# Kernel optimization log

Measured on AMD Instinct MI355X. Metric: run time of the kernel, lower is better.

Reference implementation:

```python
import jax, jax.numpy as jnp
import numpy as np

JACCARD_THRESH = 0.5
NEG_POS = 3
VAR0, VAR1 = 0.1, 0.2

def point_form(priors):
    # center form (cx,cy,w,h) -> corner form (x1,y1,x2,y2)
    return jnp.concatenate([priors[:, :2] - priors[:, 2:] / 2,
                            priors[:, :2] + priors[:, 2:] / 2], axis=1)

def jaccard(a, b):
    # a: [G,4] corner-form gt, b: [P,4] corner-form priors -> IoU [G,P]
    lt = jnp.maximum(a[:, None, :2], b[None, :, :2])
    rb = jnp.minimum(a[:, None, 2:], b[None, :, 2:])
    wh = jnp.maximum(rb - lt, 0.0)
    inter = wh[..., 0] * wh[..., 1]
    area_a = ((a[:, 2] - a[:, 0]) * (a[:, 3] - a[:, 1]))[:, None]
    area_b = ((b[:, 2] - b[:, 0]) * (b[:, 3] - b[:, 1]))[None, :]
    return inter / (area_a + area_b - inter)

def encode(matched, priors):
    # matched: [P,4] corner form; priors: [P,4] center form
    g_cxcy = ((matched[:, :2] + matched[:, 2:]) / 2 - priors[:, :2]) / (VAR0 * priors[:, 2:])
    g_wh = jnp.log((matched[:, 2:] - matched[:, :2]) / priors[:, 2:]) / VAR1
    return jnp.concatenate([g_cxcy, g_wh], axis=1)

def match_one(truths, labels, priors_c, priors_p):
    # truths: [G,4], labels: [G] -> loc_t [P,4], conf_t [P]
    G = truths.shape[0]
    overlaps = jaccard(truths, priors_p)            # [G,P]
    best_prior_idx = jnp.argmax(overlaps, axis=1)   # [G]
    best_truth_overlap = jnp.max(overlaps, axis=0)  # [P]
    best_truth_idx = jnp.argmax(overlaps, axis=0)   # [P]
    # force each gt's best prior to match that gt
    best_truth_overlap = best_truth_overlap.at[best_prior_idx].set(2.0)
    best_truth_idx = best_truth_idx.at[best_prior_idx].set(jnp.arange(G))
    matched = truths[best_truth_idx]                # [P,4]
    conf = labels[best_truth_idx].astype(jnp.int32) + 1
    conf = jnp.where(best_truth_overlap < JACCARD_THRESH, 0, conf)
    return encode(matched, priors_c), conf

def smooth_l1(x, y):
    d = jnp.abs(x - y)
    return jnp.where(d < 1.0, 0.5 * d * d, d - 0.5)

def setup_inputs() -> dict:
    key = jax.random.key(0)
    B, P, G, C = 64, 24564, 32, 81
    k1, k2, k3, k4, k5, k6, k7 = jax.random.split(key, 7)
    loc_data = jax.random.normal(k1, (B, P, 4), jnp.float32)
    conf_data = jax.random.normal(k2, (B, P, C), jnp.float32)
    # center-form priors with positive w,h
    cxcy = jax.random.uniform(k3, (P, 2), minval=0.0, maxval=1.0)
    wh = jax.random.uniform(k4, (P, 2), minval=0.05, maxval=0.5)
    dbox_list = jnp.concatenate([cxcy, wh], axis=1).astype(jnp.float32)
    # valid corner-form gt boxes + float class label in last column
    gc = jax.random.uniform(k5, (B, G, 2), minval=0.1, maxval=0.9)
    gwh = jax.random.uniform(k6, (B, G, 2), minval=0.1, maxval=0.4)
    boxes = jnp.clip(jnp.concatenate([gc - gwh / 2, gc + gwh / 2], axis=-1), 0.0, 1.0)
    labels = jax.random.randint(k7, (B, G), 0, C - 1).astype(jnp.float32)
    targets = jnp.concatenate([boxes, labels[..., None]], axis=-1).astype(jnp.float32)
    return {"loc_data": loc_data, "conf_data": conf_data,
            "dbox_list": dbox_list, "targets": targets}

def reference(loc_data, conf_data, dbox_list, targets):
    B, P, C = conf_data.shape
    priors_p = point_form(dbox_list)
    loc_t, conf_t = jax.vmap(match_one, in_axes=(0, 0, None, None))(
        targets[..., :4], targets[..., 4], dbox_list, priors_p)
    loc_t = jax.lax.stop_gradient(loc_t)           # detached in torch
    pos = conf_t > 0                               # [B,P]
    # localization smooth-L1, summed over positives
    loss_l = jnp.sum(jnp.where(pos[..., None], smooth_l1(loc_data, loc_t), 0.0))
    # per-box cross entropy
    logp = jax.nn.log_softmax(conf_data, axis=-1)  # [B,P,C]
    ce = -jnp.take_along_axis(logp, conf_t[..., None], axis=-1)[..., 0]  # [B,P]
    # hard negative mining via double argsort rank trick
    loss_for_rank = jnp.where(pos, 0.0, ce)
    loss_idx = jnp.argsort(-loss_for_rank, axis=1)
    idx_rank = jnp.argsort(loss_idx, axis=1)
    num_pos = jnp.sum(pos, axis=1, keepdims=True)  # [B,1]
    num_neg = jnp.minimum(num_pos * NEG_POS, P)
    neg = idx_rank < num_neg
    loss_c = jnp.sum(jnp.where(pos | neg, ce, 0.0))
    N = jnp.sum(num_pos).astype(loc_data.dtype)
    return loss_c / N, loss_l / N
```

## Files before the change

kernel.cpp:

```cpp
#include <hip/hip_runtime.h>
#include <math.h>


constexpr float kJT = 0.5f;
constexpr float kV0 = 0.1f;
constexpr float kV1 = 0.2f;

__global__ void init_ws_kernel(unsigned int* ws, int nwords) {
  int i = blockIdx.x * blockDim.x + threadIdx.x;
  if (i < nwords) ws[i] = 0u;
}

__global__ void match_kernel(const float* __restrict__ dbox,
                             const float* __restrict__ targets,
                             float* __restrict__ bto,
                             int* __restrict__ bti,
                             unsigned long long* __restrict__ gt_best,
                             int P, int G) {
#pragma clang fp contract(off)
  constexpr int NP = 6;
  const int b = blockIdx.y;
  const int tid = threadIdx.x;
  const int lane = tid & 63;
  const int p0 = blockIdx.x * (NP * 256);

  __shared__ float tx1[64], ty1[64], tx2[64], ty2[64], tarea[64];
  __shared__ unsigned long long sbest[64];
  if (tid < G) {
    const float* t = targets + ((size_t)b * G + tid) * 5;
    float x1 = t[0], y1 = t[1], x2 = t[2], y2 = t[3];
    tx1[tid] = x1; ty1[tid] = y1; tx2[tid] = x2; ty2[tid] = y2;
    tarea[tid] = (x2 - x1) * (y2 - y1);
    sbest[tid] = 0ull;
  }
  __syncthreads();

  float px1[NP], py1[NP], px2[NP], py2[NP], pa[NP], bov[NP];
  int bg[NP], pidx[NP];
  bool val[NP];
#pragma unroll
  for (int i = 0; i < NP; ++i) {
    int p = p0 + i * 256 + tid;
    pidx[i] = p; val[i] = (p < P);
    bov[i] = -1.0f; bg[i] = 0;
    if (val[i]) {
      const float* d = dbox + (size_t)p * 4;
      float cx = d[0], cy = d[1], w = d[2], h = d[3];
      px1[i] = cx - w * 0.5f; py1[i] = cy - h * 0.5f;
      px2[i] = cx + w * 0.5f; py2[i] = cy + h * 0.5f;
      pa[i] = (px2[i] - px1[i]) * (py2[i] - py1[i]);
    }
  }

  for (int g = 0; g < G; ++g) {
    float x1 = tx1[g], y1 = ty1[g], x2 = tx2[g], y2 = ty2[g], ta = tarea[g];
    unsigned long long lk = 0ull;
#pragma unroll
    for (int i = 0; i < NP; ++i) {
      if (!val[i]) continue;
      float lx = fmaxf(x1, px1[i]);
      float ly = fmaxf(y1, py1[i]);
      float rx = fminf(x2, px2[i]);
      float ry = fminf(y2, py2[i]);
      float w = fmaxf(rx - lx, 0.0f);
      float h = fmaxf(ry - ly, 0.0f);
      float inter = w * h;
      float ov = inter / (ta + pa[i] - inter);
      if (ov > bov[i]) { bov[i] = ov; bg[i] = g; }
      unsigned long long key =
          ((unsigned long long)__float_as_uint(ov) << 32) | (unsigned)(~(unsigned)pidx[i]);
      lk = (key > lk) ? key : lk;
    }
#pragma unroll
    for (int off = 32; off > 0; off >>= 1) {
      unsigned long long o = __shfl_xor(lk, off);
      lk = (o > lk) ? o : lk;
    }
    if (lane == 0) atomicMax(&sbest[g], lk);
  }
  __syncthreads();
  if (tid < G) atomicMax(&gt_best[(size_t)b * G + tid], sbest[tid]);

#pragma unroll
  for (int i = 0; i < NP; ++i) {
    if (val[i]) {
      bto[(size_t)b * P + pidx[i]] = bov[i];
      bti[(size_t)b * P + pidx[i]] = bg[i];
    }
  }
}

__global__ void force_kernel(const unsigned long long* __restrict__ gt_best,
                             float* __restrict__ bto, int* __restrict__ bti,
                             int P, int G, int B) {
  int b = blockIdx.x * blockDim.x + threadIdx.x;
  if (b >= B) return;
  for (int g = 0; g < G; ++g) {
    unsigned long long key = gt_best[(size_t)b * G + g];
    unsigned p = ~(unsigned)(key & 0xFFFFFFFFull);
    bto[(size_t)b * P + p] = 2.0f;
    bti[(size_t)b * P + p] = g;
  }
}

__global__ __launch_bounds__(256)
void ce_kernel(const float* __restrict__ conf,
               const float* __restrict__ loc,
               const float* __restrict__ dbox,
               const float* __restrict__ targets,
               const float* __restrict__ bto,
               const int* __restrict__ bti,
               float* __restrict__ lfr,
               int* __restrict__ num_pos,
               float* __restrict__ loss_l_b,
               float* __restrict__ ce_pos_b,
               int P, int C, int G) {
  constexpr int NC = 21;
  const int b = blockIdx.y;
  const int p0 = blockIdx.x * 64;
  const int rows = min(64, P - p0);
  const int nflt = rows * C;

  __shared__ float srow[64 * 84];
  __shared__ float s_ll, s_ce;
  __shared__ int s_np;
  if (threadIdx.x == 0) { s_ll = 0.0f; s_ce = 0.0f; s_np = 0; }

  const float* base = conf + ((size_t)b * P + p0) * (size_t)C;
  if (((uintptr_t)base & 15) == 0) {
    const float4* src4 = (const float4*)base;
    float4* dst4 = (float4*)srow;
    const int n4 = nflt >> 2;
    for (int i = threadIdx.x; i < n4; i += 256) dst4[i] = src4[i];
    for (int i = (n4 << 2) + threadIdx.x; i < nflt; i += 256) srow[i] = base[i];
  } else {
    for (int i = threadIdx.x; i < nflt; i += 256) srow[i] = base[i];
  }
  __syncthreads();

  const int lane = threadIdx.x & 63;
  const int wave = threadIdx.x >> 6;
  const int group = lane >> 2;
  const int sub = lane & 3;
  const int r = wave * 16 + group;

  if (r < rows) {
    const int p = p0 + r;
    const float* row = srow + r * C;
    float v[NC];
#pragma unroll
    for (int j = 0; j < NC; ++j) {
      int idx = j * 4 + sub;
      v[j] = (idx < C) ? row[idx] : -INFINITY;
    }
    float m = v[0];
#pragma unroll
    for (int j = 1; j < NC; ++j) m = fmaxf(m, v[j]);
    m = fmaxf(m, __shfl_xor(m, 1));
    m = fmaxf(m, __shfl_xor(m, 2));

    float s = 0.0f;
#pragma unroll
    for (int j = 0; j < NC; ++j) s += __expf(v[j] - m);
    s += __shfl_xor(s, 1);
    s += __shfl_xor(s, 2);
    float lse = m + __logf(s);

    float ov = bto[(size_t)b * P + p];
    int g = bti[(size_t)b * P + p];
    float label = targets[((size_t)b * G + g) * 5 + 4];
    int cls = (ov < kJT) ? 0 : ((int)label + 1);

    int cj = cls >> 2, cs = cls & 3;
    float vsel = 0.0f;
#pragma unroll
    for (int j = 0; j < NC; ++j) vsel = (j == cj) ? v[j] : vsel;
    float xt = (sub == cs) ? vsel : 0.0f;
    xt += __shfl_xor(xt, 1);
    xt += __shfl_xor(xt, 2);

    float ce = lse - xt;
    bool pos = cls > 0;

    if (sub == 0) {
      lfr[(size_t)b * P + p] = pos ? 0.0f : ce;
      if (pos) {
        const float* t = targets + ((size_t)b * G + g) * 5;
        float mx1 = t[0], my1 = t[1], mx2 = t[2], my2 = t[3];
        const float* d = dbox + (size_t)p * 4;
        float cx = d[0], cy = d[1], pw = d[2], ph = d[3];
        float gcx = ((mx1 + mx2) * 0.5f - cx) / (kV0 * pw);
        float gcy = ((my1 + my2) * 0.5f - cy) / (kV0 * ph);
        float gw = logf((mx2 - mx1) / pw) / kV1;
        float gh = logf((my2 - my1) / ph) / kV1;
        const float* lp = loc + ((size_t)b * P + p) * 4;
        float tloc[4] = {gcx, gcy, gw, gh};
        float ll = 0.0f;
        for (int k = 0; k < 4; ++k) {
          float dd = fabsf(lp[k] - tloc[k]);
          ll += (dd < 1.0f) ? (0.5f * dd * dd) : (dd - 0.5f);
        }
        atomicAdd(&s_ll, ll);
        atomicAdd(&s_ce, ce);
        atomicAdd(&s_np, 1);
      }
    }
  }
  __syncthreads();
  if (threadIdx.x == 0 && s_np > 0) {
    atomicAdd(&num_pos[b], s_np);
    atomicAdd(&loss_l_b[b], s_ll);
    atomicAdd(&ce_pos_b[b], s_ce);
  }
}

__global__ __launch_bounds__(1024)
void topk_kernel(const float* __restrict__ lfr,
                 const int* __restrict__ num_pos,
                 float* __restrict__ topk_sum, int P) {
  const int b = blockIdx.x;
  const int tid = threadIdx.x;
  const int lane = tid & 63;
  const int wave = tid >> 6;
  const int nthr = blockDim.x;
  const int nwav = nthr >> 6;
  const float* v = lfr + (size_t)b * P;
  int K = num_pos[b] * 3;
  if (K > P) K = P;

  __shared__ int wcnt[16][4];
  __shared__ unsigned s_prefix;
  __shared__ int s_krem;
  __shared__ float wred[16];

  if (K <= 0) {
    if (tid == 0) topk_sum[b] = 0.0f;
    return;
  }

  unsigned prefix = 0u, mask = 0u;
  int Krem = K;
  for (int shift = 30; shift >= 0; shift -= 2) {
    int c0 = 0, c1 = 0, c2 = 0, c3 = 0;
    for (int p = tid; p < P; p += nthr) {
      unsigned key = __float_as_uint(v[p]);
      bool act = (key & mask) == prefix;
      int d = (key >> shift) & 3;
      c0 += __popcll(__ballot(act & (d == 0)));
      c1 += __popcll(__ballot(act & (d == 1)));
      c2 += __popcll(__ballot(act & (d == 2)));
      c3 += __popcll(__ballot(act & (d == 3)));
    }
    if (lane == 0) {
      wcnt[wave][0] = c0; wcnt[wave][1] = c1;
      wcnt[wave][2] = c2; wcnt[wave][3] = c3;
    }
    __syncthreads();
    if (tid == 0) {
      int t[4] = {0, 0, 0, 0};
      for (int w = 0; w < nwav; ++w)
        for (int d = 0; d < 4; ++d) t[d] += wcnt[w][d];
      int run = 0, sel = 0;
      for (int d = 3; d >= 0; --d) {
        if (run + t[d] >= Krem) { sel = d; break; }
        run += t[d];
      }
      s_prefix = prefix | ((unsigned)sel << shift);
      s_krem = Krem - run;
    }
    __syncthreads();
    prefix = s_prefix;
    Krem = s_krem;
    mask |= (3u << shift);
    __syncthreads();
  }

  float Tval = __uint_as_float(prefix);
  float part = 0.0f;
  for (int p = tid; p < P; p += nthr) {
    unsigned key = __float_as_uint(v[p]);
    if (key > prefix) part += v[p];
  }
#pragma unroll
  for (int o = 1; o < 64; o <<= 1) part += __shfl_xor(part, o);
  if (lane == 0) wred[wave] = part;
  __syncthreads();
  if (tid == 0) {
    float tot = 0.0f;
    for (int w = 0; w < nwav; ++w) tot += wred[w];
    topk_sum[b] = tot + (float)Krem * Tval;
  }
}

__global__ void finalize_kernel(const int* __restrict__ num_pos,
                                const float* __restrict__ topk_sum,
                                const float* __restrict__ loss_l_b,
                                const float* __restrict__ ce_pos_b,
                                float* __restrict__ out, int B) {
  if (blockIdx.x == 0 && threadIdx.x == 0) {
    float N = 0.0f, lc = 0.0f, ll = 0.0f;
    for (int b = 0; b < B; ++b) {
      N += (float)num_pos[b];
      lc += ce_pos_b[b] + topk_sum[b];
      ll += loss_l_b[b];
    }
    out[0] = lc / N;
    out[1] = ll / N;
  }
}

extern "C" void kernel_launch(void* const* d_in, const int* in_sizes, int n_in,
                              void* d_out, int out_size, void* d_ws, size_t ws_size,
                              hipStream_t stream) {
  const float* loc = (const float*)d_in[0];
  const float* conf = (const float*)d_in[1];
  const float* dbox = (const float*)d_in[2];
  const float* targets = (const float*)d_in[3];

  const int P = in_sizes[2] / 4;
  const int B = in_sizes[0] / (P * 4);
  const int C = (int)((long long)in_sizes[1] / ((long long)B * P));
  const int G = (int)((long long)in_sizes[3] / ((long long)B * 5));

  char* ws = (char*)d_ws;
  int* num_pos = (int*)ws;
  float* topk = (float*)(ws + (size_t)B * 4);
  float* loss_l_b = (float*)(ws + (size_t)B * 8);
  float* ce_pos_b = (float*)(ws + (size_t)B * 12);
  unsigned long long* gt_best = (unsigned long long*)(ws + (size_t)B * 16);
  size_t off = (size_t)B * 16 + (size_t)B * G * 8;
  float* bto = (float*)(ws + off); off += (size_t)B * P * 4;
  int* bti = (int*)(ws + off);     off += (size_t)B * P * 4;
  float* lfr = (float*)(ws + off); off += (size_t)B * P * 4;

  int zwords = (int)(((size_t)B * 16 + (size_t)B * G * 8) / 4);
  init_ws_kernel<<<(zwords + 255) / 256, 256, 0, stream>>>((unsigned int*)d_ws, zwords);

  dim3 gA((P + 6 * 256 - 1) / (6 * 256), B);
  match_kernel<<<gA, 256, 0, stream>>>(dbox, targets, bto, bti, gt_best, P, G);

  force_kernel<<<(B + 63) / 64, 64, 0, stream>>>(gt_best, bto, bti, P, G, B);

  dim3 gC((P + 63) / 64, B);
  ce_kernel<<<gC, 256, 0, stream>>>(conf, loc, dbox, targets, bto, bti, lfr,
                                    num_pos, loss_l_b, ce_pos_b, P, C, G);

  topk_kernel<<<B, 1024, 0, stream>>>(lfr, num_pos, topk, P);

  finalize_kernel<<<1, 64, 0, stream>>>(num_pos, topk, loss_l_b, ce_pos_b,
                                        (float*)d_out, B);
}
```

Baseline: 974.8 us.

## Recompute per-prior best-truth IoU inside CE kernel and drop force kernel

The match kernel now only computes each ground truth's best prior. It no longer writes per-prior best overlap and index arrays, and the separate force kernel is removed. The CE kernel recomputes each prior's IoU against all G truths using 4 lanes per row, applies the forced match by comparing against the gt_best prior indices, and writes lfr through a lane shuffle. This removes 2×B×P×4-byte writes and reads plus one launch, in exchange for duplicated IoU arithmetic and a hardcoded G≤32 limit in shared arrays.

```diff
diff --git a/kernel.cpp b/kernel.cpp
--- a/kernel.cpp
+++ b/kernel.cpp
@@ -6,6 +6,19 @@
 constexpr float kV0 = 0.1f;
 constexpr float kV1 = 0.2f;
 
+__device__ __forceinline__ float iou_cf(float x1, float y1, float x2, float y2, float ta,
+                                        float qx1, float qy1, float qx2, float qy2, float pa) {
+#pragma clang fp contract(off)
+  float lx = fmaxf(x1, qx1);
+  float ly = fmaxf(y1, qy1);
+  float rx = fminf(x2, qx2);
+  float ry = fminf(y2, qy2);
+  float w = fmaxf(rx - lx, 0.0f);
+  float h = fmaxf(ry - ly, 0.0f);
+  float inter = w * h;
+  return inter / (ta + pa - inter);
+}
+
 __global__ void init_ws_kernel(unsigned int* ws, int nwords) {
   int i = blockIdx.x * blockDim.x + threadIdx.x;
   if (i < nwords) ws[i] = 0u;
@@ -13,8 +26,6 @@
 
 __global__ void match_kernel(const float* __restrict__ dbox,
                              const float* __restrict__ targets,
-                             float* __restrict__ bto,
-                             int* __restrict__ bti,
                              unsigned long long* __restrict__ gt_best,
                              int P, int G) {
 #pragma clang fp contract(off)
@@ -24,8 +35,8 @@
   const int lane = tid & 63;
   const int p0 = blockIdx.x * (NP * 256);
 
-  __shared__ float tx1[64], ty1[64], tx2[64], ty2[64], tarea[64];
-  __shared__ unsigned long long sbest[64];
+  __shared__ float tx1[32], ty1[32], tx2[32], ty2[32], tarea[32];
+  __shared__ unsigned long long sbest[32];
   if (tid < G) {
     const float* t = targets + ((size_t)b * G + tid) * 5;
     float x1 = t[0], y1 = t[1], x2 = t[2], y2 = t[3];
@@ -35,14 +46,13 @@
   }
   __syncthreads();
 
-  float px1[NP], py1[NP], px2[NP], py2[NP], pa[NP], bov[NP];
-  int bg[NP], pidx[NP];
+  float px1[NP], py1[NP], px2[NP], py2[NP], pa[NP];
+  int pidx[NP];
   bool val[NP];
 #pragma unroll
   for (int i = 0; i < NP; ++i) {
     int p = p0 + i * 256 + tid;
     pidx[i] = p; val[i] = (p < P);
-    bov[i] = -1.0f; bg[i] = 0;
     if (val[i]) {
       const float* d = dbox + (size_t)p * 4;
       float cx = d[0], cy = d[1], w = d[2], h = d[3];
@@ -58,15 +68,7 @@
 #pragma unroll
     for (int i = 0; i < NP; ++i) {
       if (!val[i]) continue;
-      float lx = fmaxf(x1, px1[i]);
-      float ly = fmaxf(y1, py1[i]);
-      float rx = fminf(x2, px2[i]);
-      float ry = fminf(y2, py2[i]);
-      float w = fmaxf(rx - lx, 0.0f);
-      float h = fmaxf(ry - ly, 0.0f);
-      float inter = w * h;
-      float ov = inter / (ta + pa[i] - inter);
-      if (ov > bov[i]) { bov[i] = ov; bg[i] = g; }
+      float ov = iou_cf(x1, y1, x2, y2, ta, px1[i], py1[i], px2[i], py2[i], pa[i]);
       unsigned long long key =
           ((unsigned long long)__float_as_uint(ov) << 32) | (unsigned)(~(unsigned)pidx[i]);
       lk = (key > lk) ? key : lk;
@@ -80,27 +82,6 @@
   }
   __syncthreads();
   if (tid < G) atomicMax(&gt_best[(size_t)b * G + tid], sbest[tid]);
-
-#pragma unroll
-  for (int i = 0; i < NP; ++i) {
-    if (val[i]) {
-      bto[(size_t)b * P + pidx[i]] = bov[i];
-      bti[(size_t)b * P + pidx[i]] = bg[i];
-    }
-  }
-}
-
-__global__ void force_kernel(const unsigned long long* __restrict__ gt_best,
-                             float* __restrict__ bto, int* __restrict__ bti,
-                             int P, int G, int B) {
-  int b = blockIdx.x * blockDim.x + threadIdx.x;
-  if (b >= B) return;
-  for (int g = 0; g < G; ++g) {
-    unsigned long long key = gt_best[(size_t)b * G + g];
-    unsigned p = ~(unsigned)(key & 0xFFFFFFFFull);
-    bto[(size_t)b * P + p] = 2.0f;
-    bti[(size_t)b * P + p] = g;
-  }
 }
 
 __global__ __launch_bounds__(256)
@@ -108,42 +89,69 @@
                const float* __restrict__ loc,
                const float* __restrict__ dbox,
                const float* __restrict__ targets,
-               const float* __restrict__ bto,
-               const int* __restrict__ bti,
+               const unsigned long long* __restrict__ gt_best,
                float* __restrict__ lfr,
                int* __restrict__ num_pos,
                float* __restrict__ loss_l_b,
                float* __restrict__ ce_pos_b,
                int P, int C, int G) {
+#pragma clang fp contract(off)
   constexpr int NC = 21;
   const int b = blockIdx.y;
   const int p0 = blockIdx.x * 64;
   const int rows = min(64, P - p0);
-  const int nflt = rows * C;
+  const int tid = threadIdx.x;
 
   __shared__ float srow[64 * 84];
+  __shared__ float spx1[64], spy1[64], spx2[64], spy2[64], spa[64];
+  __shared__ float spcx[64], spcy[64], spw[64], sph[64];
+  __shared__ float sgx1[32], sgy1[32], sgx2[32], sgy2[32], sga[32], slab[32];
+  __shared__ unsigned sgbp[32];
   __shared__ float s_ll, s_ce;
   __shared__ int s_np;
-  if (threadIdx.x == 0) { s_ll = 0.0f; s_ce = 0.0f; s_np = 0; }
+
+  if (tid == 0) { s_ll = 0.0f; s_ce = 0.0f; s_np = 0; }
+  if (tid < rows) {
+    const float* d = dbox + (size_t)(p0 + tid) * 4;
+    float cx = d[0], cy = d[1], w = d[2], h = d[3];
+    float x1 = cx - w * 0.5f, y1 = cy - h * 0.5f;
+    float x2 = cx + w * 0.5f, y2 = cy + h * 0.5f;
+    spx1[tid] = x1; spy1[tid] = y1; spx2[tid] = x2; spy2[tid] = y2;
+    spa[tid] = (x2 - x1) * (y2 - y1);
+    spcx[tid] = cx; spcy[tid] = cy; spw[tid] = w; sph[tid] = h;
+  }
+  if (tid >= 64 && tid < 64 + G) {
+    int g = tid - 64;
+    const float* t = targets + ((size_t)b * G + g) * 5;
+    float x1 = t[0], y1 = t[1], x2 = t[2], y2 = t[3];
+    sgx1[g] = x1; sgy1[g] = y1; sgx2[g] = x2; sgy2[g] = y2;
+    sga[g] = (x2 - x1) * (y2 - y1);
+    slab[g] = t[4];
+  }
+  if (tid >= 96 && tid < 96 + G) {
+    int g = tid - 96;
+    sgbp[g] = ~(unsigned)(gt_best[(size_t)b * G + g] & 0xFFFFFFFFull);
+  }
 
   const float* base = conf + ((size_t)b * P + p0) * (size_t)C;
-  if (((uintptr_t)base & 15) == 0) {
+  const int nflt = rows * C;
+  if ((((uintptr_t)base & 15) == 0) && ((nflt & 3) == 0)) {
     const float4* src4 = (const float4*)base;
     float4* dst4 = (float4*)srow;
     const int n4 = nflt >> 2;
-    for (int i = threadIdx.x; i < n4; i += 256) dst4[i] = src4[i];
-    for (int i = (n4 << 2) + threadIdx.x; i < nflt; i += 256) srow[i] = base[i];
+    for (int i = tid; i < n4; i += 256) dst4[i] = src4[i];
   } else {
-    for (int i = threadIdx.x; i < nflt; i += 256) srow[i] = base[i];
-  }
-  __syncthreads();
-
-  const int lane = threadIdx.x & 63;
-  const int wave = threadIdx.x >> 6;
+    for (int i = tid; i < nflt; i += 256) srow[i] = base[i];
+  }
+  __syncthreads();
+
+  const int lane = tid & 63;
+  const int wave = tid >> 6;
   const int group = lane >> 2;
   const int sub = lane & 3;
   const int r = wave * 16 + group;
 
+  float outv = 0.0f;
   if (r < rows) {
     const int p = p0 + r;
     const float* row = srow + r * C;
@@ -166,10 +174,42 @@
     s += __shfl_xor(s, 2);
     float lse = m + __logf(s);
 
-    float ov = bto[(size_t)b * P + p];
-    int g = bti[(size_t)b * P + p];
-    float label = targets[((size_t)b * G + g) * 5 + 4];
-    int cls = (ov < kJT) ? 0 : ((int)label + 1);
+    float qx1 = spx1[r], qy1 = spy1[r], qx2 = spx2[r], qy2 = spy2[r], qpa = spa[r];
+    unsigned long long kmax = 0ull;
+#pragma unroll
+    for (int j = 0; j < 8; ++j) {
+      int g = j * 4 + sub;
+      if (g < G) {
+        float ov = iou_cf(sgx1[g], sgy1[g], sgx2[g], sgy2[g], sga[g],
+                          qx1, qy1, qx2, qy2, qpa);
+        unsigned long long key =
+            ((unsigned long long)__float_as_uint(ov) << 32) | (unsigned)(~(unsigned)g);
+        kmax = (key > kmax) ? key : kmax;
+      }
+    }
+    {
+      unsigned long long o = __shfl_xor(kmax, 1);
+      kmax = (o > kmax) ? o : kmax;
+      o = __shfl_xor(kmax, 2);
+      kmax = (o > kmax) ? o : kmax;
+    }
+    int bg = (int)(~(unsigned)(kmax & 0xFFFFFFFFull));
+    float bov = __uint_as_float((unsigned)(kmax >> 32));
+
+    int fg = -1;
+#pragma unroll
+    for (int j = 0; j < 8; ++j) {
+      int g = j * 4 + sub;
+      if (g < G && sgbp[g] == (unsigned)p) fg = g;
+    }
+    fg = max(fg, __shfl_xor(fg, 1));
+    fg = max(fg, __shfl_xor(fg, 2));
+
+    float ov; int g;
+    if (fg >= 0) { ov = 2.0f; g = fg; }
+    else         { ov = bov;  g = bg; }
+
+    int cls = (ov < kJT) ? 0 : ((int)slab[g] + 1);
 
     int cj = cls >> 2, cs = cls & 3;
     float vsel = 0.0f;
@@ -181,33 +221,37 @@
 
     float ce = lse - xt;
     bool pos = cls > 0;
-
-    if (sub == 0) {
-      lfr[(size_t)b * P + p] = pos ? 0.0f : ce;
-      if (pos) {
-        const float* t = targets + ((size_t)b * G + g) * 5;
-        float mx1 = t[0], my1 = t[1], mx2 = t[2], my2 = t[3];
-        const float* d = dbox + (size_t)p * 4;
-        float cx = d[0], cy = d[1], pw = d[2], ph = d[3];
-        float gcx = ((mx1 + mx2) * 0.5f - cx) / (kV0 * pw);
-        float gcy = ((my1 + my2) * 0.5f - cy) / (kV0 * ph);
-        float gw = logf((mx2 - mx1) / pw) / kV1;
-        float gh = logf((my2 - my1) / ph) / kV1;
-        const float* lp = loc + ((size_t)b * P + p) * 4;
-        float tloc[4] = {gcx, gcy, gw, gh};
-        float ll = 0.0f;
-        for (int k = 0; k < 4; ++k) {
-          float dd = fabsf(lp[k] - tloc[k]);
-          ll += (dd < 1.0f) ? (0.5f * dd * dd) : (dd - 0.5f);
-        }
-        atomicAdd(&s_ll, ll);
-        atomicAdd(&s_ce, ce);
-        atomicAdd(&s_np, 1);
+    outv = pos ? 0.0f : ce;
+
+    if (sub == 0 && pos) {
+      float mx1 = sgx1[g], my1 = sgy1[g], mx2 = sgx2[g], my2 = sgy2[g];
+      float cx = spcx[r], cy = spcy[r], pw = spw[r], ph = sph[r];
+      float gcx = ((mx1 + mx2) * 0.5f - cx) / (kV0 * pw);
+      float gcy = ((my1 + my2) * 0.5f - cy) / (kV0 * ph);
+      float gw = logf((mx2 - mx1) / pw) / kV1;
+      float gh = logf((my2 - my1) / ph) / kV1;
+      const float* lp = loc + ((size_t)b * P + p) * 4;
+      float tloc[4] = {gcx, gcy, gw, gh};
+      float ll = 0.0f;
+      for (int k = 0; k < 4; ++k) {
+        float dd = fabsf(lp[k] - tloc[k]);
+        ll += (dd < 1.0f) ? (0.5f * dd * dd) : (dd - 0.5f);
       }
-    }
-  }
-  __syncthreads();
-  if (threadIdx.x == 0 && s_np > 0) {
+      atomicAdd(&s_ll, ll);
+      atomicAdd(&s_ce, ce);
+      atomicAdd(&s_np, 1);
+    }
+  }
+
+  {
+    int srcl = (lane < 16) ? (lane * 4) : 0;
+    float wv = __shfl(outv, srcl);
+    int rr = wave * 16 + lane;
+    if (lane < 16 && rr < rows) lfr[(size_t)b * P + p0 + rr] = wv;
+  }
+
+  __syncthreads();
+  if (tid == 0 && s_np > 0) {
     atomicAdd(&num_pos[b], s_np);
     atomicAdd(&loss_l_b[b], s_ll);
     atomicAdd(&ce_pos_b[b], s_ce);
@@ -328,21 +372,16 @@
   float* loss_l_b = (float*)(ws + (size_t)B * 8);
   float* ce_pos_b = (float*)(ws + (size_t)B * 12);
   unsigned long long* gt_best = (unsigned long long*)(ws + (size_t)B * 16);
-  size_t off = (size_t)B * 16 + (size_t)B * G * 8;
-  float* bto = (float*)(ws + off); off += (size_t)B * P * 4;
-  int* bti = (int*)(ws + off);     off += (size_t)B * P * 4;
-  float* lfr = (float*)(ws + off); off += (size_t)B * P * 4;
+  float* lfr = (float*)(ws + (size_t)B * 16 + (size_t)B * G * 8);
 
   int zwords = (int)(((size_t)B * 16 + (size_t)B * G * 8) / 4);
   init_ws_kernel<<<(zwords + 255) / 256, 256, 0, stream>>>((unsigned int*)d_ws, zwords);
 
   dim3 gA((P + 6 * 256 - 1) / (6 * 256), B);
-  match_kernel<<<gA, 256, 0, stream>>>(dbox, targets, bto, bti, gt_best, P, G);
-
-  force_kernel<<<(B + 63) / 64, 64, 0, stream>>>(gt_best, bto, bti, P, G, B);
+  match_kernel<<<gA, 256, 0, stream>>>(dbox, targets, gt_best, P, G);
 
   dim3 gC((P + 63) / 64, B);
-  ce_kernel<<<gC, 256, 0, stream>>>(conf, loc, dbox, targets, bto, bti, lfr,
+  ce_kernel<<<gC, 256, 0, stream>>>(conf, loc, dbox, targets, gt_best, lfr,
                                     num_pos, loss_l_b, ce_pos_b, P, C, G);
 
   topk_kernel<<<B, 1024, 0, stream>>>(lfr, num_pos, topk, P);
```

Result: no change. 956.5 us (-1.9%).
